# Optimization experiments

Measured on AMD Instinct MI355X. Metric: run time of the kernel, lower is better.

Reference implementation:

```python
import jax, jax.numpy as jnp
import numpy as np

B, SD, AD, M, MAXC = 65536, 32, 1, 32, 2  # batch, state_dim, action_dim, msg_dim, max_children


def _l2norm(x):
    # F.normalize(x, dim=-1) with eps=1e-12
    return x / jnp.maximum(jnp.linalg.norm(x, axis=-1, keepdims=True), 1e-12)


def _mlp(x, w1, b1, w2, b2, w3, b3):
    # MLPBase: Linear->ReLU->Linear->ReLU->Linear (400/300 hidden)
    h = jax.nn.relu(x @ w1 + b1)
    h = jax.nn.relu(h @ w2 + b2)
    return h @ w3 + b3


def setup_inputs() -> dict:
    key = jax.random.key(0)
    ks = iter(jax.random.split(key, 40))

    def p(shape):
        return jax.random.normal(next(ks), shape, jnp.float32) * 0.05

    inp = {
        "state": jax.random.normal(next(ks), (B, SD), jnp.float32),
        "action": jax.random.normal(next(ks), (B, AD), jnp.float32),
        # CriticUp params
        "up_fc1_w": p((SD + AD, 64)), "up_fc1_b": p((64,)),
        "up_fc2_w": p((64 + M, 64)), "up_fc2_b": p((64,)),
        "up_fc3_w": p((64, M)), "up_fc3_b": p((M,)),
        "att_w": p((9 + SD, M)), "att_b": p((M,)),
    }
    q_in = 12 + M + AD + M   # rel_pos(12) + self_input(msg_dim) + action + msg_down
    m_in = 12 + M + M        # rel_pos(12) + self_input + msg_down
    for n, d, out in (("q1", q_in, 1), ("q2", q_in, 1), ("msg", m_in, M * MAXC)):
        inp[n + "_w1"] = p((d, 400)); inp[n + "_b1"] = p((400,))
        inp[n + "_w2"] = p((400, 300)); inp[n + "_b2"] = p((300,))
        inp[n + "_w3"] = p((300, out)); inp[n + "_b3"] = p((out,))
    return inp


def reference(state, action,
              up_fc1_w, up_fc1_b, up_fc2_w, up_fc2_b, up_fc3_w, up_fc3_b,
              att_w, att_b,
              q1_w1, q1_b1, q1_w2, q1_b2, q1_w3, q1_b3,
              q2_w1, q2_b1, q2_w2, q2_b2, q2_w3, q2_b3,
              msg_w1, msg_b1, msg_w2, msg_b2, msg_w3, msg_b3):
    b = state.shape[0]
    # ---- bottom-up (num_limbs=1: root has no children -> zero child states/messages) ----
    xu = _l2norm(jnp.concatenate([state, action], -1) @ up_fc1_w + up_fc1_b)  # [b,64]
    ch_states = jnp.zeros((b, MAXC, 9 + SD), state.dtype)
    att = jax.nn.softmax(ch_states @ att_w + att_b, axis=-2)                  # [b,MAXC,M]
    m_up = (jnp.zeros((b, MAXC, M), state.dtype) * att).sum(-2)              # [b,M] (zeros)
    h = jnp.tanh(jnp.concatenate([xu, m_up], -1))
    h = jnp.tanh(h @ up_fc2_w + up_fc2_b)
    msg_up = _l2norm(h @ up_fc3_w + up_fc3_b)                                 # [b,M]
    # ---- top-down (root's parent index -1 wraps to itself -> zero relative offsets) ----
    pos = state[:, :3]
    rel = jnp.concatenate([jnp.zeros((b, 6), state.dtype), pos, pos], -1)     # [b,12]
    m_td = jnp.zeros((b, M), state.dtype)                                     # sliced from zero parent_msg
    xum = jnp.concatenate([rel, msg_up, action, m_td], -1)
    x1 = _mlp(xum, q1_w1, q1_b1, q1_w2, q1_b2, q1_w3, q1_b3)                  # [b,1]
    x2 = _mlp(xum, q2_w1, q2_b1, q2_w2, q2_b2, q2_w3, q2_b3)                  # [b,1]
    xm = jnp.tanh(jnp.concatenate([rel, msg_up, m_td], -1))
    msg_down = _l2norm(_mlp(xm, msg_w1, msg_b1, msg_w2, msg_b2, msg_w3, msg_b3))
    del msg_down  # computed per torch forward but unused in single-limb output
    # stack over 1 limb then sum over limb dim == identity
    return (x1, x2)
```

## Files before the change

kernel.cpp:

```cpp
#include <hip/hip_runtime.h>
#include <math.h>


#define BTOT   65536
#define XUM_OFF 655360ull

#define PK_BLK  78
#define PH_THR  512
#define PH_ROWS 128
#define PH_BLK  (BTOT / PH_ROWS)
#define F1W 0
#define F1B 2112
#define F2W 2176
#define F2B 6272
#define F3W 6336
#define F3B 8384
#define W0_FLOATS 8416

#define ML_THR  1024
#define ML_ROWS 128
#define ML_BLK  (BTOT / ML_ROWS)
#define H1S     428

typedef float  f32x4 __attribute__((ext_vector_type(4)));
typedef __bf16 bf16x8 __attribute__((ext_vector_type(8)));
typedef unsigned short u16x8 __attribute__((ext_vector_type(8)));
typedef unsigned short u16x4 __attribute__((ext_vector_type(4)));
typedef unsigned int   u32x2 __attribute__((ext_vector_type(2)));

__device__ __forceinline__ unsigned short f2b(float f) {
  union { float f; unsigned int u; } v; v.f = f;
  return (unsigned short)((v.u + 0x7fffu + ((v.u >> 16) & 1u)) >> 16);
}
__device__ __forceinline__ float b2f(unsigned short u) {
  union { unsigned int u; float f; } v; v.u = ((unsigned int)u) << 16;
  return v.f;
}
__device__ __forceinline__ f32x4 MFMA(bf16x8 a, bf16x8 b, f32x4 c) {
  return __builtin_amdgcn_mfma_f32_16x16x32_bf16(a, b, c, 0, 0, 0);
}
__device__ __forceinline__ bf16x8 ld8(const unsigned short* p) {
  return __builtin_bit_cast(bf16x8, *(const u16x8*)p);
}
__device__ __forceinline__ float ftanh(float x) {
  float e = __builtin_amdgcn_exp2f(x * 2.885390081777927f);
  return (e - 1.0f) * __builtin_amdgcn_rcpf(e + 1.0f);
}

struct P0 {
  const float* state; const float* action;
  const float* f1w; const float* f1b;
  const float* f2w; const float* f2b;
  const float* f3w; const float* f3b;
  const float* q1w1; const float* q1b1; const float* q1w2;
  const float* q2w1; const float* q2b1; const float* q2w2;
  unsigned short* ws;
  unsigned short* xum;
};

__global__ __launch_bounds__(PH_THR, 4) void phase0_kernel(P0 P) {
  __shared__ float w0[W0_FLOATS];
  __shared__ unsigned short hx[PH_ROWS * 68];
  const int tid = threadIdx.x;

  if (blockIdx.x < PK_BLK) {
    const int gid = blockIdx.x * PH_THR + tid;
    const int lane = gid & 63, f = gid >> 6;
    const int q = f / 312, fl = f - q * 312;
    const float* w1 = q ? P.q2w1 : P.q1w1;
    const float* b1 = q ? P.q2b1 : P.q1b1;
    const float* w2 = q ? P.q2w2 : P.q1w2;
    int nt, ks; const bool isw1 = (fl < 52);
    if (isw1) { nt = fl >> 1; ks = fl & 1; }
    else      { int fl2 = fl - 52; nt = fl2 / 13; ks = fl2 - nt * 13; }
    const int col = nt * 16 + (lane & 15);
    const int k0  = ks * 32 + (lane >> 4) * 8;
    unsigned short v[8];
    #pragma unroll
    for (int j = 0; j < 8; ++j) {
      const int k = k0 + j;
      float x = 0.f;
      if (isw1) {
        if (col < 400) {
          if (k < 39) x = w1[(6 + k) * 400 + col];
          else if (k == 39) x = b1[col];
        }
      } else {
        if (k < 400 && col < 300) x = w2[k * 300 + col];
      }
      v[j] = f2b(x);
    }
    *(u16x8*)(P.ws + (size_t)f * 512 + lane * 8) = *(const u16x8*)v;
    return;
  }

  const int row = tid >> 2, sub = tid & 3, j0 = sub * 16;
  const long grow = (long)(blockIdx.x - PK_BLK) * PH_ROWS + row;

  for (int i = tid; i < 528;  i += PH_THR) *(f32x4*)(w0 + F1W + 4*i) = *(const f32x4*)(P.f1w + 4*i);
  for (int i = tid; i < 16;   i += PH_THR) *(f32x4*)(w0 + F1B + 4*i) = *(const f32x4*)(P.f1b + 4*i);
  for (int i = tid; i < 1024; i += PH_THR) *(f32x4*)(w0 + F2W + 4*i) = *(const f32x4*)(P.f2w + 4*i);
  for (int i = tid; i < 16;   i += PH_THR) *(f32x4*)(w0 + F2B + 4*i) = *(const f32x4*)(P.f2b + 4*i);
  for (int i = tid; i < 512;  i += PH_THR) *(f32x4*)(w0 + F3W + 4*i) = *(const f32x4*)(P.f3w + 4*i);
  for (int i = tid; i < 8;    i += PH_THR) *(f32x4*)(w0 + F3B + 4*i) = *(const f32x4*)(P.f3b + 4*i);

  float sa[33];
  {
    const float4* sp = (const float4*)(P.state + grow * 32);
    #pragma unroll
    for (int c = 0; c < 8; ++c) {
      float4 v = sp[c];
      sa[c*4+0] = v.x; sa[c*4+1] = v.y; sa[c*4+2] = v.z; sa[c*4+3] = v.w;
    }
    sa[32] = P.action[grow];
  }
  __syncthreads();

  float acc[16];
  #pragma unroll
  for (int j = 0; j < 16; ++j) acc[j] = w0[F1B + j0 + j];
  #pragma unroll 4
  for (int i = 0; i < 33; ++i) {
    const float s = sa[i];
    const f32x4* wr = (const f32x4*)&w0[F1W + i * 64 + j0];
    #pragma unroll
    for (int c = 0; c < 4; ++c) {
      f32x4 wv = wr[c];
      acc[c*4+0] += s * wv[0]; acc[c*4+1] += s * wv[1];
      acc[c*4+2] += s * wv[2]; acc[c*4+3] += s * wv[3];
    }
  }
  {
    float ss = 0.f;
    #pragma unroll
    for (int j = 0; j < 16; ++j) ss += acc[j] * acc[j];
    ss += __shfl_xor(ss, 1, 64); ss += __shfl_xor(ss, 2, 64);
    const float sc = 1.f / fmaxf(sqrtf(ss), 1e-12f);
    #pragma unroll
    for (int j = 0; j < 16; ++j) hx[row * 68 + j0 + j] = f2b(ftanh(acc[j] * sc));
  }
  __syncthreads();
  #pragma unroll
  for (int j = 0; j < 16; ++j) acc[j] = w0[F2B + j0 + j];
  #pragma unroll 4
  for (int i0 = 0; i0 < 16; ++i0) {
    const u16x4 hv4 = *(const u16x4*)&hx[row * 68 + i0 * 4];
    #pragma unroll
    for (int u = 0; u < 4; ++u) {
      const float hv = b2f(hv4[u]);
      const f32x4* wr = (const f32x4*)&w0[F2W + (i0 * 4 + u) * 64 + j0];
      #pragma unroll
      for (int c = 0; c < 4; ++c) {
        f32x4 wv = wr[c];
        acc[c*4+0] += hv * wv[0]; acc[c*4+1] += hv * wv[1];
        acc[c*4+2] += hv * wv[2]; acc[c*4+3] += hv * wv[3];
      }
    }
  }
  __syncthreads();
  #pragma unroll
  for (int j = 0; j < 16; ++j) hx[row * 68 + j0 + j] = f2b(ftanh(acc[j]));
  __syncthreads();
  const int j0m = sub * 8;
  float am[8];
  #pragma unroll
  for (int j = 0; j < 8; ++j) am[j] = w0[F3B + j0m + j];
  #pragma unroll 4
  for (int i0 = 0; i0 < 16; ++i0) {
    const u16x4 hv4 = *(const u16x4*)&hx[row * 68 + i0 * 4];
    #pragma unroll
    for (int u = 0; u < 4; ++u) {
      const float hv = b2f(hv4[u]);
      const f32x4* wr = (const f32x4*)&w0[F3W + (i0 * 4 + u) * 32 + j0m];
      #pragma unroll
      for (int c = 0; c < 2; ++c) {
        f32x4 wv = wr[c];
        am[c*4+0] += hv * wv[0]; am[c*4+1] += hv * wv[1];
        am[c*4+2] += hv * wv[2]; am[c*4+3] += hv * wv[3];
      }
    }
  }
  float sm = 0.f;
  #pragma unroll
  for (int j = 0; j < 8; ++j) sm += am[j] * am[j];
  sm += __shfl_xor(sm, 1, 64); sm += __shfl_xor(sm, 2, 64);
  const float scm = 1.f / fmaxf(sqrtf(sm), 1e-12f);
  __syncthreads();
  #pragma unroll
  for (int j = 0; j < 8; ++j) hx[row * 68 + j0m + j] = f2b(am[j] * scm);
  __syncthreads();
  {
    u16x8 v0, v1;
    #pragma unroll
    for (int t = 0; t < 16; ++t) {
      const int c = j0 + t;
      unsigned short u;
      if      (c < 3)  u = f2b(sa[c]);
      else if (c < 6)  u = f2b(sa[c - 3]);
      else if (c < 38) u = hx[row * 68 + (c - 6)];
      else if (c == 38) u = f2b(sa[32]);
      else if (c == 39) u = 0x3f80;
      else              u = 0;
      if (t < 8) v0[t] = u; else v1[t - 8] = u;
    }
    unsigned short* dst = P.xum + (size_t)grow * 64 + j0;
    *(u16x8*)dst = v0;
    *(u16x8*)(dst + 8) = v1;
  }
}

struct P1 {
  const unsigned short* img; const unsigned short* xum;
  const float* q1b2; const float* q1w3; const float* q1b3;
  const float* q2b2; const float* q2w3; const float* q2b3;
  float* out;
};

__global__ __launch_bounds__(ML_THR) void mlp_kernel(P1 P) {
  __shared__ __align__(16) unsigned short h1[ML_ROWS * H1S];
  __shared__ float xred[ML_ROWS * 4];

  const int tid  = threadIdx.x;
  const int lane = tid & 63, w = tid >> 6;
  const int rl = lane & 15, g = lane >> 4;

  const int r1 = w & 7, ch = w >> 3;
  const int wm = w >> 2, wn = w & 3;

  const unsigned short* xr = P.xum + ((size_t)blockIdx.x * ML_ROWS + r1 * 16 + rl) * 64;
  const bf16x8 af0 = ld8(xr + g * 8);
  const bf16x8 af1 = ld8(xr + 32 + g * 8);

  for (int q = 0; q < 2; ++q) {
    {
      const unsigned short* w1f = P.img + ((size_t)(q * 312 + ch * 26)) * 512 + lane * 8;
      unsigned short* h1w = &h1[(size_t)(r1 * 16 + rl) * H1S + ch * 208 + g * 4];
      bf16x8 wA0 = ld8(w1f + 0 * 512), wA1 = ld8(w1f + 1 * 512);
      bf16x8 wB0 = ld8(w1f + 2 * 512), wB1 = ld8(w1f + 3 * 512);
      for (int t = 0; t < 13; t += 2) {
        {
          f32x4 a = (f32x4){0.f, 0.f, 0.f, 0.f};
          a = MFMA(wA0, af0, a);
          a = MFMA(wA1, af1, a);
          if (t + 2 < 13) {
            wA0 = ld8(w1f + (size_t)((t + 2) * 2) * 512);
            wA1 = ld8(w1f + (size_t)((t + 2) * 2 + 1) * 512);
          }
          const float c0 = fmaxf(a[0], 0.f), c1 = fmaxf(a[1], 0.f);
          const float c2 = fmaxf(a[2], 0.f), c3 = fmaxf(a[3], 0.f);
          unsigned int p01, p23;
          asm("v_cvt_pk_bf16_f32 %0, %1, %2" : "=v"(p01) : "v"(c0), "v"(c1));
          asm("v_cvt_pk_bf16_f32 %0, %1, %2" : "=v"(p23) : "v"(c2), "v"(c3));
          u32x2 pk; pk[0] = p01; pk[1] = p23;
          *(u32x2*)(h1w + t * 16) = pk;
        }
        if (t + 1 < 13) {
          f32x4 a = (f32x4){0.f, 0.f, 0.f, 0.f};
          a = MFMA(wB0, af0, a);
          a = MFMA(wB1, af1, a);
          if (t + 3 < 13) {
            wB0 = ld8(w1f + (size_t)((t + 3) * 2) * 512);
            wB1 = ld8(w1f + (size_t)((t + 3) * 2 + 1) * 512);
          }
          const float c0 = fmaxf(a[0], 0.f), c1 = fmaxf(a[1], 0.f);
          const float c2 = fmaxf(a[2], 0.f), c3 = fmaxf(a[3], 0.f);
          unsigned int p01, p23;
          asm("v_cvt_pk_bf16_f32 %0, %1, %2" : "=v"(p01) : "v"(c0), "v"(c1));
          asm("v_cvt_pk_bf16_f32 %0, %1, %2" : "=v"(p23) : "v"(c2), "v"(c3));
          u32x2 pk; pk[0] = p01; pk[1] = p23;
          *(u32x2*)(h1w + (t + 1) * 16) = pk;
        }
      }
    }
    __syncthreads();

    f32x4 acc2[2][5];
    #pragma unroll
    for (int mt = 0; mt < 2; ++mt)
      #pragma unroll
      for (int jn = 0; jn < 5; ++jn) acc2[mt][jn] = (f32x4){0.f, 0.f, 0.f, 0.f};
    {
      const unsigned short* w2f = P.img + ((size_t)(q * 312 + 52 + wn * 65)) * 512 + lane * 8;
      bf16x8 bA[5], bB[5];
      #pragma unroll
      for (int jn = 0; jn < 5; ++jn) bA[jn] = ld8(w2f + (size_t)(jn * 13 + 0) * 512);
      #pragma unroll
      for (int jn = 0; jn < 5; ++jn) bB[jn] = ld8(w2f + (size_t)(jn * 13 + 1) * 512);
      for (int ks = 0; ks < 13; ks += 2) {
        {
          const bf16x8 a0 = ld8(&h1[(size_t)(wm * 32 + rl) * H1S + ks * 32 + g * 8]);
          const bf16x8 a1 = ld8(&h1[(size_t)(wm * 32 + 16 + rl) * H1S + ks * 32 + g * 8]);
          #pragma unroll
          for (int jn = 0; jn < 5; ++jn) {
            acc2[0][jn] = MFMA(a0, bA[jn], acc2[0][jn]);
            acc2[1][jn] = MFMA(a1, bA[jn], acc2[1][jn]);
          }
          if (ks + 2 < 13) {
            #pragma unroll
            for (int jn = 0; jn < 5; ++jn)
              bA[jn] = ld8(w2f + (size_t)(jn * 13 + ks + 2) * 512);
          }
        }
        if (ks + 1 < 13) {
          const bf16x8 a0 = ld8(&h1[(size_t)(wm * 32 + rl) * H1S + (ks + 1) * 32 + g * 8]);
          const bf16x8 a1 = ld8(&h1[(size_t)(wm * 32 + 16 + rl) * H1S + (ks + 1) * 32 + g * 8]);
          #pragma unroll
          for (int jn = 0; jn < 5; ++jn) {
            acc2[0][jn] = MFMA(a0, bB[jn], acc2[0][jn]);
            acc2[1][jn] = MFMA(a1, bB[jn], acc2[1][jn]);
          }
          if (ks + 3 < 13) {
            #pragma unroll
            for (int jn = 0; jn < 5; ++jn)
              bB[jn] = ld8(w2f + (size_t)(jn * 13 + ks + 3) * 512);
          }
        }
      }
    }

    const float* b2p = q ? P.q2b2 : P.q1b2;
    const float* w3  = q ? P.q2w3 : P.q1w3;
    const float* b3  = q ? P.q2b3 : P.q1b3;
    float xp[2][4];
    #pragma unroll
    for (int mt = 0; mt < 2; ++mt)
      #pragma unroll
      for (int i = 0; i < 4; ++i) xp[mt][i] = 0.f;
    #pragma unroll
    for (int jn = 0; jn < 5; ++jn) {
      const int n = wn * 80 + jn * 16 + rl;
      if (n < 300) {
        const float bv = b2p[n], wv = w3[n];
        #pragma unroll
        for (int mt = 0; mt < 2; ++mt)
          #pragma unroll
          for (int i = 0; i < 4; ++i)
            xp[mt][i] += fmaxf(acc2[mt][jn][i] + bv, 0.f) * wv;
      }
    }
    #pragma unroll
    for (int off = 1; off < 16; off <<= 1)
      #pragma unroll
      for (int mt = 0; mt < 2; ++mt)
        #pragma unroll
        for (int i = 0; i < 4; ++i)
          xp[mt][i] += __shfl_xor(xp[mt][i], off, 64);
    if (rl == 0) {
      #pragma unroll
      for (int mt = 0; mt < 2; ++mt)
        #pragma unroll
        for (int i = 0; i < 4; ++i)
          xred[(wm * 32 + mt * 16 + g * 4 + i) * 4 + wn] = xp[mt][i];
    }
    __syncthreads();
    if (tid < ML_ROWS) {
      const float4 xv = *(const float4*)&xred[tid * 4];
      P.out[(size_t)q * BTOT + (size_t)blockIdx.x * ML_ROWS + tid] =
          xv.x + xv.y + xv.z + xv.w + b3[0];
    }
    __syncthreads();
  }
}

extern "C" void kernel_launch(void* const* d_in, const int* in_sizes, int n_in,
                              void* d_out, int out_size, void* d_ws, size_t ws_size,
                              hipStream_t stream) {
  (void)in_sizes; (void)n_in; (void)out_size; (void)ws_size;
  P0 A;
  A.state  = (const float*)d_in[0];
  A.action = (const float*)d_in[1];
  A.f1w = (const float*)d_in[2]; A.f1b = (const float*)d_in[3];
  A.f2w = (const float*)d_in[4]; A.f2b = (const float*)d_in[5];
  A.f3w = (const float*)d_in[6]; A.f3b = (const float*)d_in[7];
  A.q1w1 = (const float*)d_in[10]; A.q1b1 = (const float*)d_in[11]; A.q1w2 = (const float*)d_in[12];
  A.q2w1 = (const float*)d_in[16]; A.q2b1 = (const float*)d_in[17]; A.q2w2 = (const float*)d_in[18];
  A.ws  = (unsigned short*)d_ws;
  A.xum = (unsigned short*)((unsigned char*)d_ws + XUM_OFF);
  phase0_kernel<<<dim3(PK_BLK + PH_BLK), dim3(PH_THR), 0, stream>>>(A);

  P1 B;
  B.img  = (const unsigned short*)d_ws;
  B.xum  = (const unsigned short*)((unsigned char*)d_ws + XUM_OFF);
  B.q1b2 = (const float*)d_in[13]; B.q1w3 = (const float*)d_in[14]; B.q1b3 = (const float*)d_in[15];
  B.q2b2 = (const float*)d_in[19]; B.q2w3 = (const float*)d_in[20]; B.q2b3 = (const float*)d_in[21];
  B.out  = (float*)d_out;
  mlp_kernel<<<dim3(ML_BLK), dim3(ML_THR), 0, stream>>>(B);
}
```

Measured before the change: 112.2 us.

## Halve MLP block threads and double per-wave row tiles for weight reuse

The MLP kernel drops from 1024 to 512 threads per block. Each wave now covers twice as many rows in both layers: two 16-row tiles in layer 1 and four in layer 2. This lets each global weight fragment load feed more MFMAs, cutting weight traffic per row. The cost is more accumulator registers per wave (20 f32x4 in layer 2), which could pressure VGPRs, and fewer waves to hide latency. Launch bounds request 2 blocks per CU.

```diff
diff --git a/kernel.cpp b/kernel.cpp
--- a/kernel.cpp
+++ b/kernel.cpp
@@ -17,7 +17,7 @@
 #define F3B 8384
 #define W0_FLOATS 8416
 
-#define ML_THR  1024
+#define ML_THR  512
 #define ML_ROWS 128
 #define ML_BLK  (BTOT / ML_ROWS)
 #define H1S     428
@@ -216,7 +216,7 @@
   float* out;
 };
 
-__global__ __launch_bounds__(ML_THR) void mlp_kernel(P1 P) {
+__global__ __launch_bounds__(ML_THR, 2) void mlp_kernel(P1 P) {
   __shared__ __align__(16) unsigned short h1[ML_ROWS * H1S];
   __shared__ float xred[ML_ROWS * 4];
 
@@ -224,59 +224,77 @@
   const int lane = tid & 63, w = tid >> 6;
   const int rl = lane & 15, g = lane >> 4;
 
-  const int r1 = w & 7, ch = w >> 3;
+  const int rp = w & 3, ch = w >> 2;
   const int wm = w >> 2, wn = w & 3;
 
-  const unsigned short* xr = P.xum + ((size_t)blockIdx.x * ML_ROWS + r1 * 16 + rl) * 64;
-  const bf16x8 af0 = ld8(xr + g * 8);
-  const bf16x8 af1 = ld8(xr + 32 + g * 8);
+  const unsigned short* xr0 = P.xum + ((size_t)blockIdx.x * ML_ROWS + rp * 32 + rl) * 64;
+  const bf16x8 af0k0 = ld8(xr0 + g * 8);
+  const bf16x8 af0k1 = ld8(xr0 + 32 + g * 8);
+  const unsigned short* xr1 = xr0 + 16 * 64;
+  const bf16x8 af1k0 = ld8(xr1 + g * 8);
+  const bf16x8 af1k1 = ld8(xr1 + 32 + g * 8);
 
   for (int q = 0; q < 2; ++q) {
     {
       const unsigned short* w1f = P.img + ((size_t)(q * 312 + ch * 26)) * 512 + lane * 8;
-      unsigned short* h1w = &h1[(size_t)(r1 * 16 + rl) * H1S + ch * 208 + g * 4];
+      unsigned short* h1w0 = &h1[(size_t)(rp * 32 + rl) * H1S + ch * 208 + g * 4];
+      unsigned short* h1w1 = &h1[(size_t)(rp * 32 + 16 + rl) * H1S + ch * 208 + g * 4];
       bf16x8 wA0 = ld8(w1f + 0 * 512), wA1 = ld8(w1f + 1 * 512);
       bf16x8 wB0 = ld8(w1f + 2 * 512), wB1 = ld8(w1f + 3 * 512);
       for (int t = 0; t < 13; t += 2) {
         {
           f32x4 a = (f32x4){0.f, 0.f, 0.f, 0.f};
-          a = MFMA(wA0, af0, a);
-          a = MFMA(wA1, af1, a);
+          f32x4 b = (f32x4){0.f, 0.f, 0.f, 0.f};
+          a = MFMA(wA0, af0k0, a); a = MFMA(wA1, af0k1, a);
+          b = MFMA(wA0, af1k0, b); b = MFMA(wA1, af1k1, b);
           if (t + 2 < 13) {
             wA0 = ld8(w1f + (size_t)((t + 2) * 2) * 512);
             wA1 = ld8(w1f + (size_t)((t + 2) * 2 + 1) * 512);
           }
-          const float c0 = fmaxf(a[0], 0.f), c1 = fmaxf(a[1], 0.f);
-          const float c2 = fmaxf(a[2], 0.f), c3 = fmaxf(a[3], 0.f);
-          unsigned int p01, p23;
-          asm("v_cvt_pk_bf16_f32 %0, %1, %2" : "=v"(p01) : "v"(c0), "v"(c1));
-          asm("v_cvt_pk_bf16_f32 %0, %1, %2" : "=v"(p23) : "v"(c2), "v"(c3));
+          unsigned int p01, p23, q01, q23;
+          const float a0 = fmaxf(a[0], 0.f), a1 = fmaxf(a[1], 0.f);
+          const float a2 = fmaxf(a[2], 0.f), a3 = fmaxf(a[3], 0.f);
+          const float b0 = fmaxf(b[0], 0.f), b1 = fmaxf(b[1], 0.f);
+          const float b2 = fmaxf(b[2], 0.f), b3 = fmaxf(b[3], 0.f);
+          asm("v_cvt_pk_bf16_f32 %0, %1, %2" : "=v"(p01) : "v"(a0), "v"(a1));
+          asm("v_cvt_pk_bf16_f32 %0, %1, %2" : "=v"(p23) : "v"(a2), "v"(a3));
+          asm("v_cvt_pk_bf16_f32 %0, %1, %2" : "=v"(q01) : "v"(b0), "v"(b1));
+          asm("v_cvt_pk_bf16_f32 %0, %1, %2" : "=v"(q23) : "v"(b2), "v"(b3));
           u32x2 pk; pk[0] = p01; pk[1] = p23;
-          *(u32x2*)(h1w + t * 16) = pk;
+          u32x2 qk; qk[0] = q01; qk[1] = q23;
+          *(u32x2*)(h1w0 + t * 16) = pk;
+          *(u32x2*)(h1w1 + t * 16) = qk;
         }
         if (t + 1 < 13) {
           f32x4 a = (f32x4){0.f, 0.f, 0.f, 0.f};
-          a = MFMA(wB0, af0, a);
-          a = MFMA(wB1, af1, a);
+          f32x4 b = (f32x4){0.f, 0.f, 0.f, 0.f};
+          a = MFMA(wB0, af0k0, a); a = MFMA(wB1, af0k1, a);
+          b = MFMA(wB0, af1k0, b); b = MFMA(wB1, af1k1, b);
           if (t + 3 < 13) {
             wB0 = ld8(w1f + (size_t)((t + 3) * 2) * 512);
             wB1 = ld8(w1f + (size_t)((t + 3) * 2 + 1) * 512);
           }
-          const float c0 = fmaxf(a[0], 0.f), c1 = fmaxf(a[1], 0.f);
-          const float c2 = fmaxf(a[2], 0.f), c3 = fmaxf(a[3], 0.f);
-          unsigned int p01, p23;
-          asm("v_cvt_pk_bf16_f32 %0, %1, %2" : "=v"(p01) : "v"(c0), "v"(c1));
-          asm("v_cvt_pk_bf16_f32 %0, %1, %2" : "=v"(p23) : "v"(c2), "v"(c3));
+          unsigned int p01, p23, q01, q23;
+          const float a0 = fmaxf(a[0], 0.f), a1 = fmaxf(a[1], 0.f);
+          const float a2 = fmaxf(a[2], 0.f), a3 = fmaxf(a[3], 0.f);
+          const float b0 = fmaxf(b[0], 0.f), b1 = fmaxf(b[1], 0.f);
+          const float b2 = fmaxf(b[2], 0.f), b3 = fmaxf(b[3], 0.f);
+          asm("v_cvt_pk_bf16_f32 %0, %1, %2" : "=v"(p01) : "v"(a0), "v"(a1));
+          asm("v_cvt_pk_bf16_f32 %0, %1, %2" : "=v"(p23) : "v"(a2), "v"(a3));
+          asm("v_cvt_pk_bf16_f32 %0, %1, %2" : "=v"(q01) : "v"(b0), "v"(b1));
+          asm("v_cvt_pk_bf16_f32 %0, %1, %2" : "=v"(q23) : "v"(b2), "v"(b3));
           u32x2 pk; pk[0] = p01; pk[1] = p23;
-          *(u32x2*)(h1w + (t + 1) * 16) = pk;
+          u32x2 qk; qk[0] = q01; qk[1] = q23;
+          *(u32x2*)(h1w0 + (t + 1) * 16) = pk;
+          *(u32x2*)(h1w1 + (t + 1) * 16) = qk;
         }
       }
     }
     __syncthreads();
 
-    f32x4 acc2[2][5];
-    #pragma unroll
-    for (int mt = 0; mt < 2; ++mt)
+    f32x4 acc2[4][5];
+    #pragma unroll
+    for (int mt = 0; mt < 4; ++mt)
       #pragma unroll
       for (int jn = 0; jn < 5; ++jn) acc2[mt][jn] = (f32x4){0.f, 0.f, 0.f, 0.f};
     {
@@ -288,13 +306,15 @@
       for (int jn = 0; jn < 5; ++jn) bB[jn] = ld8(w2f + (size_t)(jn * 13 + 1) * 512);
       for (int ks = 0; ks < 13; ks += 2) {
         {
-          const bf16x8 a0 = ld8(&h1[(size_t)(wm * 32 + rl) * H1S + ks * 32 + g * 8]);
-          const bf16x8 a1 = ld8(&h1[(size_t)(wm * 32 + 16 + rl) * H1S + ks * 32 + g * 8]);
+          bf16x8 am[4];
           #pragma unroll
-          for (int jn = 0; jn < 5; ++jn) {
-            acc2[0][jn] = MFMA(a0, bA[jn], acc2[0][jn]);
-            acc2[1][jn] = MFMA(a1, bA[jn], acc2[1][jn]);
-          }
+          for (int mt = 0; mt < 4; ++mt)
+            am[mt] = ld8(&h1[(size_t)(wm * 64 + mt * 16 + rl) * H1S + ks * 32 + g * 8]);
+          #pragma unroll
+          for (int jn = 0; jn < 5; ++jn)
+            #pragma unroll
+            for (int mt = 0; mt < 4; ++mt)
+              acc2[mt][jn] = MFMA(am[mt], bA[jn], acc2[mt][jn]);
           if (ks + 2 < 13) {
             #pragma unroll
             for (int jn = 0; jn < 5; ++jn)
@@ -302,13 +322,15 @@
           }
         }
         if (ks + 1 < 13) {
-          const bf16x8 a0 = ld8(&h1[(size_t)(wm * 32 + rl) * H1S + (ks + 1) * 32 + g * 8]);
-          const bf16x8 a1 = ld8(&h1[(size_t)(wm * 32 + 16 + rl) * H1S + (ks + 1) * 32 + g * 8]);
+          bf16x8 am[4];
           #pragma unroll
-          for (int jn = 0; jn < 5; ++jn) {
-            acc2[0][jn] = MFMA(a0, bB[jn], acc2[0][jn]);
-            acc2[1][jn] = MFMA(a1, bB[jn], acc2[1][jn]);
-          }
+          for (int mt = 0; mt < 4; ++mt)
+            am[mt] = ld8(&h1[(size_t)(wm * 64 + mt * 16 + rl) * H1S + (ks + 1) * 32 + g * 8]);
+          #pragma unroll
+          for (int jn = 0; jn < 5; ++jn)
+            #pragma unroll
+            for (int mt = 0; mt < 4; ++mt)
+              acc2[mt][jn] = MFMA(am[mt], bB[jn], acc2[mt][jn]);
           if (ks + 3 < 13) {
             #pragma unroll
             for (int jn = 0; jn < 5; ++jn)
@@ -321,9 +343,9 @@
     const float* b2p = q ? P.q2b2 : P.q1b2;
     const float* w3  = q ? P.q2w3 : P.q1w3;
     const float* b3  = q ? P.q2b3 : P.q1b3;
-    float xp[2][4];
-    #pragma unroll
-    for (int mt = 0; mt < 2; ++mt)
+    float xp[4][4];
+    #pragma unroll
+    for (int mt = 0; mt < 4; ++mt)
       #pragma unroll
       for (int i = 0; i < 4; ++i) xp[mt][i] = 0.f;
     #pragma unroll
@@ -332,7 +354,7 @@
       if (n < 300) {
         const float bv = b2p[n], wv = w3[n];
         #pragma unroll
-        for (int mt = 0; mt < 2; ++mt)
+        for (int mt = 0; mt < 4; ++mt)
           #pragma unroll
           for (int i = 0; i < 4; ++i)
             xp[mt][i] += fmaxf(acc2[mt][jn][i] + bv, 0.f) * wv;
@@ -341,16 +363,16 @@
     #pragma unroll
     for (int off = 1; off < 16; off <<= 1)
       #pragma unroll
-      for (int mt = 0; mt < 2; ++mt)
+      for (int mt = 0; mt < 4; ++mt)
         #pragma unroll
         for (int i = 0; i < 4; ++i)
           xp[mt][i] += __shfl_xor(xp[mt][i], off, 64);
     if (rl == 0) {
       #pragma unroll
-      for (int mt = 0; mt < 2; ++mt)
+      for (int mt = 0; mt < 4; ++mt)
         #pragma unroll
         for (int i = 0; i < 4; ++i)
-          xred[(wm * 32 + mt * 16 + g * 4 + i) * 4 + wn] = xp[mt][i];
+          xred[(wm * 64 + mt * 16 + g * 4 + i) * 4 + wn] = xp[mt][i];
     }
     __syncthreads();
     if (tid < ML_ROWS) {
```

Measured after the change: 104.4 us (median of 2 runs). -6.9%, faster.
